# Performance work log

Hardware: AMD Instinct MI355X
Metric: run time of the kernel (lower is better)

## Reference

```python
import jax, jax.numpy as jnp
import numpy as np

D_MODEL = 1024
N_HEADS = 16
HEAD_DIM = D_MODEL // N_HEADS
BATCH = 2
SEQ = 2048


def setup_inputs() -> dict:
    key = jax.random.key(0)
    ks = jax.random.split(key, 7)
    s = 1.0 / np.sqrt(D_MODEL)
    return {
        "x": jax.random.normal(ks[0], (BATCH, SEQ, D_MODEL), dtype=jnp.float32),
        "Wq": jax.random.normal(ks[1], (D_MODEL, D_MODEL), dtype=jnp.float32) * s,
        "Wk": jax.random.normal(ks[2], (D_MODEL, D_MODEL), dtype=jnp.float32) * s,
        "Wv": jax.random.normal(ks[3], (D_MODEL, D_MODEL), dtype=jnp.float32) * s,
        "Wo": jax.random.normal(ks[4], (D_MODEL, D_MODEL), dtype=jnp.float32) * s,
        "Wg": jax.random.normal(ks[5], (D_MODEL, D_MODEL), dtype=jnp.float32) * s,
        "bg": jnp.zeros((D_MODEL,), dtype=jnp.float32),
    }


def _rope_cos_sin(seq_len, head_dim, dtype):
    half = head_dim // 2
    inv_freq = 1.0 / (10000.0 ** (jnp.arange(half, dtype=jnp.float32) / half))
    freqs = jnp.arange(seq_len, dtype=jnp.float32)[:, None] * inv_freq[None, :]  # (S, half)
    emb = jnp.concatenate([freqs, freqs], axis=-1)  # (S, head_dim)
    return jnp.cos(emb).astype(dtype), jnp.sin(emb).astype(dtype)


def _rotate_half(x):
    half = x.shape[-1] // 2
    return jnp.concatenate([-x[..., half:], x[..., :half]], axis=-1)


def reference(x, Wq, Wk, Wv, Wo, Wg, bg):
    bsz, seq_len, d_model = x.shape
    # projections (torch Linear: x @ W.T)
    q = jnp.einsum('bsd,ed->bse', x, Wq).reshape(bsz, seq_len, N_HEADS, HEAD_DIM).transpose(0, 2, 1, 3)
    k = jnp.einsum('bsd,ed->bse', x, Wk).reshape(bsz, seq_len, N_HEADS, HEAD_DIM).transpose(0, 2, 1, 3)
    v = jnp.einsum('bsd,ed->bse', x, Wv).reshape(bsz, seq_len, N_HEADS, HEAD_DIM).transpose(0, 2, 1, 3)
    cos, sin = _rope_cos_sin(seq_len, HEAD_DIM, x.dtype)  # (S, hd)
    cos = cos[None, None]
    sin = sin[None, None]
    q = q * cos + _rotate_half(q) * sin
    k = k * cos + _rotate_half(k) * sin
    scores = jnp.einsum('bhqd,bhkd->bhqk', q, k) / jnp.sqrt(jnp.asarray(HEAD_DIM, x.dtype))
    causal = jnp.triu(jnp.full((seq_len, seq_len), -jnp.inf, dtype=x.dtype), k=1)
    scores = scores + causal
    probs = jax.nn.softmax(scores, axis=-1)
    attn = jnp.einsum('bhqk,bhkd->bhqd', probs, v)  # (B,H,S,hd)
    attn = attn.transpose(0, 2, 1, 3).reshape(bsz, seq_len, d_model)
    out = jnp.einsum('bsd,ed->bse', attn, Wo)
    gate = jax.nn.sigmoid(jnp.einsum('bsd,ed->bse', out, Wg) + bg)
    return out * gate
```

## Files before the change

kernel.cpp:

```cpp
#include <hip/hip_runtime.h>

#define DM 1024
#define NH 16
#define HD 64
#define BATCH 2
#define SEQ 2048
#define MROWS (BATCH*SEQ)

typedef unsigned short u16;
typedef unsigned long long u64;
typedef __bf16 bf16x8 __attribute__((ext_vector_type(8)));
typedef float f32x4 __attribute__((ext_vector_type(4)));
typedef unsigned int u32x4 __attribute__((ext_vector_type(4)));
typedef unsigned int __attribute__((address_space(1))) as1_uint;
typedef unsigned int __attribute__((address_space(3))) as3_uint;

__device__ __forceinline__ u16 f2bf(float f) {
  unsigned u = __builtin_bit_cast(unsigned, f);
  u += 0x7fffu + ((u >> 16) & 1u);
  return (u16)(u >> 16);
}
__device__ __forceinline__ float bf2f(u16 h) {
  return __builtin_bit_cast(float, ((unsigned)h) << 16);
}
__device__ __forceinline__ bf16x8 ld8(const u16* p) {
  return __builtin_bit_cast(bf16x8, *reinterpret_cast<const u32x4*>(p));
}
__device__ __forceinline__ void gl_lds16(const u16* g, void* lds) {
  __builtin_amdgcn_global_load_lds((const as1_uint*)(const void*)g,
                                   (as3_uint*)lds, 16, 0, 0);
}
__device__ __forceinline__ unsigned pk2(float a, float b) {
  return __builtin_amdgcn_perm(__builtin_bit_cast(unsigned, a),
                               __builtin_bit_cast(unsigned, b), 0x07060302u);
}

__global__ void convall_kernel(const float* __restrict__ x,
                               const float* __restrict__ w0, const float* __restrict__ w1,
                               const float* __restrict__ w2, const float* __restrict__ w3,
                               const float* __restrict__ w4, u16* __restrict__ out) {
  const size_t NX = (size_t)MROWS * DM;
  size_t i = ((size_t)blockIdx.x * 256 + threadIdx.x) * 4;
  const float* src;
  size_t off;
  if (i < NX) { src = x; off = i; }
  else {
    size_t j = i - NX;
    int wsel = (int)(j >> 20);
    off = j & ((1u << 20) - 1);
    src = (wsel == 0) ? w0 : (wsel == 1) ? w1 : (wsel == 2) ? w2 : (wsel == 3) ? w3 : w4;
  }
  f32x4 v = *reinterpret_cast<const f32x4*>(src + off);
  out[i + 0] = f2bf(v[0]);
  out[i + 1] = f2bf(v[1]);
  out[i + 2] = f2bf(v[2]);
  out[i + 3] = f2bf(v[3]);
}

__global__ void tab_kernel(float* __restrict__ tab) {
  int t = blockIdx.x * 256 + threadIdx.x;
  if (t >= SEQ * 32) return;
  int s = t >> 5, i = t & 31;
  float inv = powf(10000.0f, -(float)i / 32.0f);
  float f = (float)s * inv;
  tab[s * 64 + i] = cosf(f);
  tab[s * 64 + 32 + i] = sinf(f);
}

__global__ __launch_bounds__(256) void qkv_gemm(
    const u16* __restrict__ A, const u16* __restrict__ Bw,
    u16* __restrict__ Qr, u16* __restrict__ Kr, u16* __restrict__ Vt,
    const float* __restrict__ tab) {
  const int z = blockIdx.z;
  const u16* B = Bw + (size_t)z * DM * DM;
  int flat = blockIdx.y * 16 + blockIdx.x;
  flat = (flat & 7) * 64 + (flat >> 3);
  const int bx = flat & 15, by = flat >> 4;
  const int m0 = by * 128;
  const int h = bx;
  const int t = threadIdx.x, w = t >> 6, l = t & 63;
  const int lr = l & 15, lg = l >> 4;
  __shared__ __align__(16) u16 SM[8704];
  u16* As = SM;
  u16* Bs = SM + 4096;
  f32x4 acc[2][4] = {};
  const int srow = t >> 2, sc8 = (t & 3) * 8;
  const u16* gA = A + (size_t)(m0 + srow) * DM + sc8;
  const u16* gB = B + (size_t)(h * 64 + srow) * DM + sc8;
  char* lA = (char*)As + w * 1024;
  char* lB = (char*)Bs + w * 1024;
  const size_t rstep = (size_t)64 * DM;

  for (int kt = 0; kt < DM; kt += 32) {
    gl_lds16(gA + kt, lA);
    gl_lds16(gA + kt + rstep, lA + 4096);
    gl_lds16(gB + kt, lB);
    __syncthreads();
    bf16x8 af[2], bfr[4];
    af[0] = ld8(&As[(w * 32 + lr) * 32 + lg * 8]);
    af[1] = ld8(&As[(w * 32 + 16 + lr) * 32 + lg * 8]);
#pragma unroll
    for (int ni = 0; ni < 4; ++ni) bfr[ni] = ld8(&Bs[(ni * 16 + lr) * 32 + lg * 8]);
#pragma unroll
    for (int mi = 0; mi < 2; ++mi)
#pragma unroll
      for (int ni = 0; ni < 4; ++ni)
        acc[mi][ni] = __builtin_amdgcn_mfma_f32_16x16x32_bf16(af[mi], bfr[ni], acc[mi][ni], 0, 0, 0);
    __syncthreads();
  }

  if (z < 2) {
    u16* Out = (z == 0) ? Qr : Kr;
#pragma unroll
    for (int mi = 0; mi < 2; ++mi)
#pragma unroll
      for (int r = 0; r < 4; ++r) {
        const int row = m0 + w * 32 + mi * 16 + lg * 4 + r;
        const int b = row >> 11, s = row & (SEQ - 1);
        const size_t ob = ((size_t)(b * NH + h) * SEQ + s) * 64;
#pragma unroll
        for (int ni = 0; ni < 2; ++ni) {
          const int i = ni * 16 + lr;
          const float c = tab[s * 64 + i], sn = tab[s * 64 + 32 + i];
          const float v1 = acc[mi][ni][r], v2 = acc[mi][ni + 2][r];
          Out[ob + i] = f2bf(v1 * c - v2 * sn);
          Out[ob + 32 + i] = f2bf(v2 * c + v1 * sn);
        }
      }
  } else {
    u16* T = SM;
#pragma unroll
    for (int mi = 0; mi < 2; ++mi)
#pragma unroll
      for (int ni = 0; ni < 4; ++ni) {
        const int cc = ni * 16 + lr;
        const int rw = w * 32 + mi * 16 + lg * 4;
#pragma unroll
        for (int r = 0; r < 4; ++r) T[cc * 136 + rw + r] = f2bf(acc[mi][ni][r]);
      }
    __syncthreads();
    const int d = t >> 2, seg = t & 3;
    const int b = m0 >> 11, sbase = (m0 & (SEQ - 1)) + seg * 32;
    u16* dst = Vt + ((size_t)(b * NH + h) * 64 + d) * SEQ + sbase;
    const u16* srcT = T + d * 136 + seg * 32;
#pragma unroll
    for (int j = 0; j < 4; ++j)
      *reinterpret_cast<u32x4*>(dst + j * 8) =
          *reinterpret_cast<const u32x4*>(srcT + j * 8);
  }
}

template <int MODE>
__global__ __launch_bounds__(256) void gemm_bt(
    const u16* __restrict__ A, const u16* __restrict__ B,
    u16* __restrict__ Cb, float* __restrict__ Cf,
    const float* __restrict__ bias, const u16* __restrict__ mult,
    int M, int N, int K) {
  const int gx = gridDim.x;
  int nwg = gx * gridDim.y;
  int flat = blockIdx.y * gx + blockIdx.x;
  flat = (flat & 7) * (nwg >> 3) + (flat >> 3);
  const int bx = flat % gx, by = flat / gx;
  A += (size_t)by * 128 * K;
  B += (size_t)bx * 64 * K;
  if constexpr (MODE == 1) Cb += (size_t)by * 128 * N + bx * 64;
  if constexpr (MODE == 2) {
    Cf += (size_t)by * 128 * N + bx * 64;
    bias += bx * 64;
    mult += (size_t)by * 128 * N + bx * 64;
  }
  const int t = threadIdx.x, w = t >> 6;
  const int l = t & 63;
  const int wr = w >> 1, wc = w & 1;
  const int lr = l & 15, lg = l >> 4;
  __shared__ __align__(16) u16 As[128 * 32];
  __shared__ __align__(16) u16 Bs[64 * 32];
  f32x4 acc[4][2] = {};
  const int srow = t >> 2;
  const int sc8 = (t & 3) * 8;
  const u16* gA = A + (size_t)srow * K + sc8;
  const u16* gB = B + (size_t)srow * K + sc8;
  char* lA = (char*)As + w * 1024;
  char* lB = (char*)Bs + w * 1024;
  const size_t rstep = (size_t)64 * K;

  for (int kt = 0; kt < K; kt += 32) {
    gl_lds16(gA + kt, lA);
    gl_lds16(gA + kt + rstep, lA + 4096);
    gl_lds16(gB + kt, lB);
    __syncthreads();
    bf16x8 af[4], bfr[2];
#pragma unroll
    for (int i = 0; i < 4; ++i)
      af[i] = ld8(&As[(wr * 64 + i * 16 + lr) * 32 + lg * 8]);
#pragma unroll
    for (int i = 0; i < 2; ++i)
      bfr[i] = ld8(&Bs[(wc * 32 + i * 16 + lr) * 32 + lg * 8]);
#pragma unroll
    for (int mi = 0; mi < 4; ++mi)
#pragma unroll
      for (int ni = 0; ni < 2; ++ni)
        acc[mi][ni] = __builtin_amdgcn_mfma_f32_16x16x32_bf16(af[mi], bfr[ni], acc[mi][ni], 0, 0, 0);
    __syncthreads();
  }
#pragma unroll
  for (int mi = 0; mi < 4; ++mi)
#pragma unroll
    for (int ni = 0; ni < 2; ++ni)
#pragma unroll
      for (int r = 0; r < 4; ++r) {
        int row = wr * 64 + mi * 16 + lg * 4 + r;
        int col = wc * 32 + ni * 16 + lr;
        size_t idx = (size_t)row * N + col;
        float v = acc[mi][ni][r];
        if constexpr (MODE == 1) {
          Cb[idx] = f2bf(v);
        } else {
          float g = 1.0f / (1.0f + __expf(-(v + bias[col])));
          Cf[idx] = bf2f(mult[idx]) * g;
        }
      }
}

__global__ __launch_bounds__(128) void attn_kernel(
    const u16* __restrict__ Q, const u16* __restrict__ K, const u16* __restrict__ Vt,
    u16* __restrict__ O) {
  const int f = blockIdx.x;
  const int rank = f >> 3;
  const int bh = (f & 7) * 4 + (rank & 3);
  const int j = rank >> 2;
  const int u = j & 7, v = j >> 3;
  const int qb = (v == 0) ? (31 - u) : (v == 1) ? (16 + u) : (v == 2) ? (15 - u) : u;

  const int t = threadIdx.x, w = t >> 6, l = t & 63;
  const int lr = l & 15, lg = l >> 4;
  const int qw0 = qb * 64 + w * 32;
  const size_t base = (size_t)bh * SEQ * 64;
  const size_t vbase = (size_t)bh * 64 * SEQ;
  __shared__ __align__(16) u16 Ks[2][64 * 64];
  __shared__ __align__(16) u16 Ps[2][2][1024];

  bf16x8 qf[2][2];
#pragma unroll
  for (int qs = 0; qs < 2; ++qs) {
    const u16* qp = &Q[base + (size_t)(qw0 + qs * 16 + lr) * 64 + lg * 8];
    qf[qs][0] = ld8(qp);
    qf[qs][1] = ld8(qp + 32);
  }

  f32x4 oacc[2][4] = {};
  float l_part[2] = {0.0f, 0.0f};
  const int nt = qb + 1;

#define STAGE_K(tile) do { const int kv_ = (tile) * 64; u16* kb_ = Ks[(tile) & 1];   \
    _Pragma("unroll") for (int c_ = 0; c_ < 4; ++c_) {                               \
      const int row_ = w * 32 + c_ * 8 + (l >> 3);                                   \
      const int slot_ = (l & 7) ^ (row_ & 7);                                        \
      gl_lds16(K + base + (size_t)(kv_ + row_) * 64 + slot_ * 8,                     \
               (char*)kb_ + (w * 32 + c_ * 8) * 128);                                \
    } } while (0)

  STAGE_K(0);
  __syncthreads();

  for (int tk = 0; tk < nt; ++tk) {
    const int kv0 = tk * 64;
    const char* kb = (const char*)Ks[tk & 1];
    bf16x8 vf[2][4];
#pragma unroll
    for (int ks = 0; ks < 2; ++ks)
#pragma unroll
      for (int dc = 0; dc < 4; ++dc)
        vf[ks][dc] = ld8(&Vt[vbase + (size_t)(dc * 16 + lr) * SEQ + kv0 + ks * 32 + lg * 8]);
    if (tk + 1 < nt) STAGE_K(tk + 1);

    bf16x8 kf[4][2];
    const int swk = lr & 7;
#pragma unroll
    for (int h = 0; h < 4; ++h) {
      const char* rp = kb + (h * 16 + lr) * 128;
      kf[h][0] = *(const bf16x8*)(rp + ((lg ^ swk) << 4));
      kf[h][1] = *(const bf16x8*)(rp + (((4 + lg) ^ swk) << 4));
    }
    const int swz = (lr & 7) << 4;
#pragma unroll
    for (int qs = 0; qs < 2; ++qs) {
      const int qs0 = qw0 + qs * 16;
      f32x4 st[4];
#pragma unroll
      for (int h = 0; h < 4; ++h) {
        f32x4 z = {};
        z = __builtin_amdgcn_mfma_f32_16x16x32_bf16(kf[h][0], qf[qs][0], z, 0, 0, 0);
        z = __builtin_amdgcn_mfma_f32_16x16x32_bf16(kf[h][1], qf[qs][1], z, 0, 0, 0);
        st[h] = z;
      }
      float pv[4][4];
#pragma unroll
      for (int h = 0; h < 4; ++h)
#pragma unroll
        for (int r = 0; r < 4; ++r)
          pv[h][r] = fmaf(st[h][r], 0.1803368801f, -12.0f);
      if (tk == qb) {
#pragma unroll
        for (int h = 0; h < 4; ++h)
#pragma unroll
          for (int r = 0; r < 4; ++r)
            if (kv0 + h * 16 + lg * 4 + r > qs0 + lr) pv[h][r] = -1e30f;
      }
      float hs[4];
#pragma unroll
      for (int h = 0; h < 4; ++h) {
#pragma unroll
        for (int r = 0; r < 4; ++r) pv[h][r] = exp2f(pv[h][r]);
        hs[h] = (pv[h][0] + pv[h][1]) + (pv[h][2] + pv[h][3]);
      }
      l_part[qs] += (hs[0] + hs[1]) + (hs[2] + hs[3]);
      char* pq = (char*)Ps[w][qs];
#pragma unroll
      for (int h = 0; h < 4; ++h) {
        u64 pw = (u64)pk2(pv[h][1], pv[h][0]) | ((u64)pk2(pv[h][3], pv[h][2]) << 32);
        *(u64*)(pq + ((((h >> 1) * 512 + lr * 32 + (h & 1) * 16 + lg * 4) * 2) ^ swz)) = pw;
      }
    }
#pragma unroll
    for (int ks = 0; ks < 2; ++ks) {
      bf16x8 pf[2];
#pragma unroll
      for (int qs = 0; qs < 2; ++qs)
        pf[qs] = *(const bf16x8*)((char*)Ps[w][qs] + ((ks * 1024 + lr * 64 + lg * 16) ^ swz));
#pragma unroll
      for (int dc = 0; dc < 4; ++dc)
#pragma unroll
        for (int qs = 0; qs < 2; ++qs)
          oacc[qs][dc] = __builtin_amdgcn_mfma_f32_16x16x32_bf16(pf[qs], vf[ks][dc], oacc[qs][dc], 0, 0, 0);
    }
    __syncthreads();
  }
#undef STAGE_K
  const int b = bh >> 4, hh = bh & 15;
#pragma unroll
  for (int qs = 0; qs < 2; ++qs) {
    float ls = l_part[qs];
    ls += __shfl_xor(ls, 16);
    ls += __shfl_xor(ls, 32);
    const int qs0 = qw0 + qs * 16;
#pragma unroll
    for (int r = 0; r < 4; ++r) {
      float inv = 1.0f / __shfl(ls, lg * 4 + r);
#pragma unroll
      for (int dc = 0; dc < 4; ++dc)
        O[((size_t)(b * SEQ + qs0 + lg * 4 + r)) * DM + hh * 64 + dc * 16 + lr] =
            f2bf(oacc[qs][dc][r] * inv);
    }
  }
}

extern "C" void kernel_launch(void* const* d_in, const int* in_sizes, int n_in,
                              void* d_out, int out_size, void* d_ws, size_t ws_size,
                              hipStream_t stream) {
  const float* x = (const float*)d_in[0];
  const float* Wq = (const float*)d_in[1];
  const float* Wk = (const float*)d_in[2];
  const float* Wv = (const float*)d_in[3];
  const float* Wo = (const float*)d_in[4];
  const float* Wg = (const float*)d_in[5];
  const float* bg = (const float*)d_in[6];
  float* out = (float*)d_out;

  const size_t NX = (size_t)MROWS * DM;
  const size_t NW = (size_t)DM * DM;
  u16* xbf = (u16*)d_ws;
  u16* wbf = xbf + NX;
  u16* qkvr = wbf + 5 * NW;
  u16* attn = qkvr + 3 * NX;
  u16* outbf = attn + NX;
  float* tab = (float*)(outbf + NX);

  convall_kernel<<<(NX + 5 * NW) / 1024, 256, 0, stream>>>(x, Wq, Wk, Wv, Wo, Wg, xbf);
  tab_kernel<<<(SEQ * 32) / 256, 256, 0, stream>>>(tab);
  qkv_gemm<<<dim3(16, 32, 3), 256, 0, stream>>>(
      xbf, wbf, qkvr, qkvr + NX, qkvr + 2 * NX, tab);
  attn_kernel<<<dim3(1024), 128, 0, stream>>>(
      qkvr, qkvr + NX, qkvr + 2 * NX, attn);
  gemm_bt<1><<<dim3(16, 32), 256, 0, stream>>>(
      attn, wbf + 3 * NW, outbf, nullptr, nullptr, nullptr, MROWS, DM, DM);
  gemm_bt<2><<<dim3(16, 32), 256, 0, stream>>>(
      outbf, wbf + 4 * NW, nullptr, out, bg, outbf, MROWS, DM, DM);
}
```

Baseline: 239.1 us.

## Rewrite attention with 32x32 MFMA, single-wave blocks, and register-only P

The attention kernel now runs one 64-thread wave per 32-query strip and uses 32x32x16 bf16 MFMA for both QK^T and PV. K is loaded straight from global memory into registers with a one-tile prefetch instead of being staged through LDS. P is rearranged between lane halves with cross-lane shuffles instead of round-tripping through shared memory. This removes all LDS traffic and block barriers and doubles the grid, but each wave now does its own K/V global loads with no sharing across waves, and register pressure rises.

After: 245.3 us. 1.03x slower.

```diff
diff --git a/kernel.cpp b/kernel.cpp
--- a/kernel.cpp
+++ b/kernel.cpp
@@ -11,6 +11,7 @@
 typedef unsigned long long u64;
 typedef __bf16 bf16x8 __attribute__((ext_vector_type(8)));
 typedef float f32x4 __attribute__((ext_vector_type(4)));
+typedef float f32x16 __attribute__((ext_vector_type(16)));
 typedef unsigned int u32x4 __attribute__((ext_vector_type(4)));
 typedef unsigned int __attribute__((address_space(1))) as1_uint;
 typedef unsigned int __attribute__((address_space(3))) as3_uint;
@@ -222,137 +223,136 @@
       }
 }
 
-__global__ __launch_bounds__(128) void attn_kernel(
+__global__ __launch_bounds__(64) void attn_kernel(
     const u16* __restrict__ Q, const u16* __restrict__ K, const u16* __restrict__ Vt,
     u16* __restrict__ O) {
   const int f = blockIdx.x;
-  const int rank = f >> 3;
-  const int bh = (f & 7) * 4 + (rank & 3);
-  const int j = rank >> 2;
-  const int u = j & 7, v = j >> 3;
-  const int qb = (v == 0) ? (31 - u) : (v == 1) ? (16 + u) : (v == 2) ? (15 - u) : u;
-
-  const int t = threadIdx.x, w = t >> 6, l = t & 63;
-  const int lr = l & 15, lg = l >> 4;
-  const int qw0 = qb * 64 + w * 32;
+  const int i = f >> 3;
+  const int bh = (f & 7) * 4 + (i & 3);
+  const int j = i >> 2;
+  const int u = j & 31;
+  const int strip = (j >> 5) ? u : 63 - u;
+  const int qw0 = strip * 32;
+  const int nt = (strip >> 1) + 1;
+
+  const int l = threadIdx.x;
+  const int r31 = l & 31, hi = l >> 5;
   const size_t base = (size_t)bh * SEQ * 64;
   const size_t vbase = (size_t)bh * 64 * SEQ;
-  __shared__ __align__(16) u16 Ks[2][64 * 64];
-  __shared__ __align__(16) u16 Ps[2][2][1024];
-
-  bf16x8 qf[2][2];
-#pragma unroll
-  for (int qs = 0; qs < 2; ++qs) {
-    const u16* qp = &Q[base + (size_t)(qw0 + qs * 16 + lr) * 64 + lg * 8];
-    qf[qs][0] = ld8(qp);
-    qf[qs][1] = ld8(qp + 32);
-  }
-
-  f32x4 oacc[2][4] = {};
-  float l_part[2] = {0.0f, 0.0f};
-  const int nt = qb + 1;
-
-#define STAGE_K(tile) do { const int kv_ = (tile) * 64; u16* kb_ = Ks[(tile) & 1];   \
-    _Pragma("unroll") for (int c_ = 0; c_ < 4; ++c_) {                               \
-      const int row_ = w * 32 + c_ * 8 + (l >> 3);                                   \
-      const int slot_ = (l & 7) ^ (row_ & 7);                                        \
-      gl_lds16(K + base + (size_t)(kv_ + row_) * 64 + slot_ * 8,                     \
-               (char*)kb_ + (w * 32 + c_ * 8) * 128);                                \
-    } } while (0)
-
-  STAGE_K(0);
-  __syncthreads();
+
+  bf16x8 qf[4];
+  const u16* qp = Q + base + (size_t)(qw0 + r31) * 64 + hi * 8;
+#pragma unroll
+  for (int s = 0; s < 4; ++s) qf[s] = ld8(qp + s * 16);
+
+  f32x16 oacc[2] = {};
+  float l_part = 0.0f;
+
+  const u16* Kp = K + base + (size_t)r31 * 64 + hi * 8;
+  const u16* Vp = Vt + vbase + (size_t)r31 * SEQ + hi * 8;
+
+#define LOADK(dst, tile) do { const size_t kvo_ = (size_t)(tile) * 4096;        \
+    _Pragma("unroll") for (int s_ = 0; s_ < 4; ++s_) {                          \
+      dst[0][s_] = ld8(Kp + kvo_ + s_ * 16);                                    \
+      dst[1][s_] = ld8(Kp + kvo_ + 2048 + s_ * 16); } } while (0)
+
+  bf16x8 kf[2][4], kn[2][4];
+  LOADK(kf, 0);
 
   for (int tk = 0; tk < nt; ++tk) {
     const int kv0 = tk * 64;
-    const char* kb = (const char*)Ks[tk & 1];
-    bf16x8 vf[2][4];
-#pragma unroll
-    for (int ks = 0; ks < 2; ++ks)
-#pragma unroll
-      for (int dc = 0; dc < 4; ++dc)
-        vf[ks][dc] = ld8(&Vt[vbase + (size_t)(dc * 16 + lr) * SEQ + kv0 + ks * 32 + lg * 8]);
-    if (tk + 1 < nt) STAGE_K(tk + 1);
-
-    bf16x8 kf[4][2];
-    const int swk = lr & 7;
-#pragma unroll
-    for (int h = 0; h < 4; ++h) {
-      const char* rp = kb + (h * 16 + lr) * 128;
-      kf[h][0] = *(const bf16x8*)(rp + ((lg ^ swk) << 4));
-      kf[h][1] = *(const bf16x8*)(rp + (((4 + lg) ^ swk) << 4));
-    }
-    const int swz = (lr & 7) << 4;
-#pragma unroll
-    for (int qs = 0; qs < 2; ++qs) {
-      const int qs0 = qw0 + qs * 16;
-      f32x4 st[4];
-#pragma unroll
-      for (int h = 0; h < 4; ++h) {
-        f32x4 z = {};
-        z = __builtin_amdgcn_mfma_f32_16x16x32_bf16(kf[h][0], qf[qs][0], z, 0, 0, 0);
-        z = __builtin_amdgcn_mfma_f32_16x16x32_bf16(kf[h][1], qf[qs][1], z, 0, 0, 0);
-        st[h] = z;
+    bf16x8 vf[2][2][2];
+#pragma unroll
+    for (int kvh = 0; kvh < 2; ++kvh)
+#pragma unroll
+      for (int ksl = 0; ksl < 2; ++ksl)
+#pragma unroll
+        for (int dm = 0; dm < 2; ++dm)
+          vf[kvh][ksl][dm] =
+              ld8(Vp + (size_t)dm * 32 * SEQ + kv0 + kvh * 32 + ksl * 16);
+    if (tk + 1 < nt) LOADK(kn, tk + 1);
+
+    f32x16 st[2];
+#pragma unroll
+    for (int kvh = 0; kvh < 2; ++kvh) {
+      f32x16 z{};
+#pragma unroll
+      for (int s = 0; s < 4; ++s)
+        z = __builtin_amdgcn_mfma_f32_32x32x16_bf16(kf[kvh][s], qf[s], z, 0, 0, 0);
+      st[kvh] = z;
+    }
+    float p[2][16];
+#pragma unroll
+    for (int kvh = 0; kvh < 2; ++kvh)
+#pragma unroll
+      for (int r = 0; r < 16; ++r)
+        p[kvh][r] = fmaf(st[kvh][r], 0.1803368801f, -12.0f);
+    if (tk == nt - 1) {
+#pragma unroll
+      for (int kvh = 0; kvh < 2; ++kvh)
+#pragma unroll
+        for (int r = 0; r < 16; ++r) {
+          const int kv_abs = kv0 + kvh * 32 + (r & 3) + 4 * hi + 8 * (r >> 2);
+          if (kv_abs > qw0 + r31) p[kvh][r] = -1e30f;
+        }
+    }
+    float acc_l = 0.0f;
+#pragma unroll
+    for (int kvh = 0; kvh < 2; ++kvh) {
+#pragma unroll
+      for (int r = 0; r < 16; ++r) p[kvh][r] = exp2f(p[kvh][r]);
+      float a = (p[kvh][0] + p[kvh][1]) + (p[kvh][2] + p[kvh][3]);
+      float b2 = (p[kvh][4] + p[kvh][5]) + (p[kvh][6] + p[kvh][7]);
+      float c2 = (p[kvh][8] + p[kvh][9]) + (p[kvh][10] + p[kvh][11]);
+      float d2 = (p[kvh][12] + p[kvh][13]) + (p[kvh][14] + p[kvh][15]);
+      acc_l += (a + b2) + (c2 + d2);
+    }
+    l_part += acc_l;
+#pragma unroll
+    for (int kvh = 0; kvh < 2; ++kvh) {
+      unsigned dw[8];
+#pragma unroll
+      for (int m = 0; m < 8; ++m) dw[m] = pk2(p[kvh][2 * m + 1], p[kvh][2 * m]);
+#pragma unroll
+      for (int ksl = 0; ksl < 2; ++ksl) {
+        const unsigned v0 = hi ? dw[4 * ksl + 0] : dw[4 * ksl + 2];
+        const unsigned v1 = hi ? dw[4 * ksl + 1] : dw[4 * ksl + 3];
+        const unsigned s0 = (unsigned)__shfl((int)v0, l ^ 32);
+        const unsigned s1 = (unsigned)__shfl((int)v1, l ^ 32);
+        u32x4 pw;
+        pw[0] = hi ? s0 : dw[4 * ksl + 0];
+        pw[1] = hi ? s1 : dw[4 * ksl + 1];
+        pw[2] = hi ? dw[4 * ksl + 2] : s0;
+        pw[3] = hi ? dw[4 * ksl + 3] : s1;
+        const bf16x8 pfrag = __builtin_bit_cast(bf16x8, pw);
+#pragma unroll
+        for (int dm = 0; dm < 2; ++dm)
+          oacc[dm] = __builtin_amdgcn_mfma_f32_32x32x16_bf16(
+              vf[kvh][ksl][dm], pfrag, oacc[dm], 0, 0, 0);
       }
-      float pv[4][4];
-#pragma unroll
-      for (int h = 0; h < 4; ++h)
-#pragma unroll
-        for (int r = 0; r < 4; ++r)
-          pv[h][r] = fmaf(st[h][r], 0.1803368801f, -12.0f);
-      if (tk == qb) {
-#pragma unroll
-        for (int h = 0; h < 4; ++h)
-#pragma unroll
-          for (int r = 0; r < 4; ++r)
-            if (kv0 + h * 16 + lg * 4 + r > qs0 + lr) pv[h][r] = -1e30f;
-      }
-      float hs[4];
-#pragma unroll
-      for (int h = 0; h < 4; ++h) {
-#pragma unroll
-        for (int r = 0; r < 4; ++r) pv[h][r] = exp2f(pv[h][r]);
-        hs[h] = (pv[h][0] + pv[h][1]) + (pv[h][2] + pv[h][3]);
-      }
-      l_part[qs] += (hs[0] + hs[1]) + (hs[2] + hs[3]);
-      char* pq = (char*)Ps[w][qs];
-#pragma unroll
-      for (int h = 0; h < 4; ++h) {
-        u64 pw = (u64)pk2(pv[h][1], pv[h][0]) | ((u64)pk2(pv[h][3], pv[h][2]) << 32);
-        *(u64*)(pq + ((((h >> 1) * 512 + lr * 32 + (h & 1) * 16 + lg * 4) * 2) ^ swz)) = pw;
-      }
-    }
-#pragma unroll
-    for (int ks = 0; ks < 2; ++ks) {
-      bf16x8 pf[2];
-#pragma unroll
-      for (int qs = 0; qs < 2; ++qs)
-        pf[qs] = *(const bf16x8*)((char*)Ps[w][qs] + ((ks * 1024 + lr * 64 + lg * 16) ^ swz));
-#pragma unroll
-      for (int dc = 0; dc < 4; ++dc)
-#pragma unroll
-        for (int qs = 0; qs < 2; ++qs)
-          oacc[qs][dc] = __builtin_amdgcn_mfma_f32_16x16x32_bf16(pf[qs], vf[ks][dc], oacc[qs][dc], 0, 0, 0);
-    }
-    __syncthreads();
-  }
-#undef STAGE_K
+    }
+#pragma unroll
+    for (int kvh = 0; kvh < 2; ++kvh)
+#pragma unroll
+      for (int s = 0; s < 4; ++s) kf[kvh][s] = kn[kvh][s];
+  }
+#undef LOADK
+  const float ls = l_part + __shfl_xor(l_part, 32);
+  const float inv = 1.0f / ls;
+  const int q_abs = qw0 + r31;
   const int b = bh >> 4, hh = bh & 15;
-#pragma unroll
-  for (int qs = 0; qs < 2; ++qs) {
-    float ls = l_part[qs];
-    ls += __shfl_xor(ls, 16);
-    ls += __shfl_xor(ls, 32);
-    const int qs0 = qw0 + qs * 16;
-#pragma unroll
-    for (int r = 0; r < 4; ++r) {
-      float inv = 1.0f / __shfl(ls, lg * 4 + r);
-#pragma unroll
-      for (int dc = 0; dc < 4; ++dc)
-        O[((size_t)(b * SEQ + qs0 + lg * 4 + r)) * DM + hh * 64 + dc * 16 + lr] =
-            f2bf(oacc[qs][dc][r] * inv);
-    }
-  }
+  u16* Orow = O + ((size_t)(b * SEQ + q_abs)) * DM + hh * 64;
+#pragma unroll
+  for (int dm = 0; dm < 2; ++dm)
+#pragma unroll
+    for (int rr = 0; rr < 4; ++rr) {
+      const float a0 = oacc[dm][4 * rr + 0] * inv;
+      const float a1 = oacc[dm][4 * rr + 1] * inv;
+      const float a2 = oacc[dm][4 * rr + 2] * inv;
+      const float a3 = oacc[dm][4 * rr + 3] * inv;
+      const u64 wv = (u64)pk2(a1, a0) | ((u64)pk2(a3, a2) << 32);
+      *reinterpret_cast<u64*>(Orow + dm * 32 + 8 * rr + 4 * hi) = wv;
+    }
 }
 
 extern "C" void kernel_launch(void* const* d_in, const int* in_sizes, int n_in,
@@ -380,7 +380,7 @@
   tab_kernel<<<(SEQ * 32) / 256, 256, 0, stream>>>(tab);
   qkv_gemm<<<dim3(16, 32, 3), 256, 0, stream>>>(
       xbf, wbf, qkvr, qkvr + NX, qkvr + 2 * NX, tab);
-  attn_kernel<<<dim3(1024), 128, 0, stream>>>(
+  attn_kernel<<<dim3(2048), 64, 0, stream>>>(
       qkvr, qkvr + NX, qkvr + 2 * NX, attn);
   gemm_bt<1><<<dim3(16, 32), 256, 0, stream>>>(
       attn, wbf + 3 * NW, outbf, nullptr, nullptr, nullptr, MROWS, DM, DM);
```
